# Performance work log

Hardware: AMD Instinct MI355X
Metric: run time of the kernel (lower is better)

The kernel has to match this reference:

```python
import jax, jax.numpy as jnp
import numpy as np

N = 100000   # nodes
E = 1600000  # edges (avg degree 16)
D = 64       # input feature dim


def _lin(k, i, o):
    return (jax.random.normal(k, (i, o), jnp.float32) / np.float32(np.sqrt(i)))


def setup_inputs() -> dict:
    key = jax.random.key(0)
    ks = jax.random.split(key, 12)
    return {
        "x": jax.random.normal(ks[0], (N, D), jnp.float32),
        "edge_index": jax.random.randint(ks[1], (2, E), 0, N, dtype=jnp.int64),
        # layer 1: SAGEConv(64, 64, 'pool')
        "W1_pool": _lin(ks[2], 64, 64), "b1_pool": jnp.zeros((64,), jnp.float32),
        "W1_self": _lin(ks[3], 64, 64), "W1_neigh": _lin(ks[4], 64, 64),
        "b1": jnp.zeros((64,), jnp.float32),
        # layer 2: SAGEConv(64, 32, 'pool')
        "W2_pool": _lin(ks[5], 64, 64), "b2_pool": jnp.zeros((64,), jnp.float32),
        "W2_self": _lin(ks[6], 64, 32), "W2_neigh": _lin(ks[7], 64, 32),
        "b2": jnp.zeros((32,), jnp.float32),
        # layer 3: SAGEConv(32, 32, 'mean')
        "W3_self": _lin(ks[8], 32, 32), "W3_neigh": _lin(ks[9], 32, 32),
        "b3": jnp.zeros((32,), jnp.float32),
    }


def _sage_pool(x, src, dst, Wp, bp, Ws, Wn, b):
    # max-pool aggregator: transform all nodes once (cheaper than per-edge),
    # gather per-edge, segment-max into destination nodes.
    m = jax.nn.relu(x @ Wp + bp)[src]                      # [E, in]
    agg = jax.ops.segment_max(m, dst, num_segments=N)     # [N, in]
    agg = jnp.where(jnp.isfinite(agg), agg, jnp.float32(0.0))  # isolated nodes -> 0
    return x @ Ws + agg @ Wn + b


def _sage_mean(x, src, dst, Ws, Wn, b):
    s = jax.ops.segment_sum(x[src], dst, num_segments=N)   # [N, in]
    cnt = jax.ops.segment_sum(jnp.ones((src.shape[0],), jnp.float32), dst,
                              num_segments=N)
    agg = s / jnp.maximum(cnt, jnp.float32(1.0))[:, None]
    return x @ Ws + agg @ Wn + b


def reference(x, edge_index,
              W1_pool, b1_pool, W1_self, W1_neigh, b1,
              W2_pool, b2_pool, W2_self, W2_neigh, b2,
              W3_self, W3_neigh, b3):
    src, dst = edge_index[0], edge_index[1]
    h = jax.nn.relu(_sage_pool(x, src, dst, W1_pool, b1_pool, W1_self, W1_neigh, b1))
    h = _sage_pool(h, src, dst, W2_pool, b2_pool, W2_self, W2_neigh, b2)
    h = _sage_mean(h, src, dst, W3_self, W3_neigh, b3)
    return h
```

## Files before the change

### kernel.cpp

```cpp
#include <hip/hip_runtime.h>
#include <hip/hip_bf16.h>


typedef unsigned int uint;
typedef short short8 __attribute__((ext_vector_type(8)));
typedef float f32x4 __attribute__((ext_vector_type(4)));
typedef float f32x2 __attribute__((ext_vector_type(2)));
typedef unsigned short u16x8 __attribute__((ext_vector_type(8)));

__device__ __forceinline__ float bf2f(unsigned short h){
  return __uint_as_float(((uint)h) << 16);
}
__device__ __forceinline__ unsigned short f2bf(float f){
  uint u = __float_as_uint(f);
  u += 0x7fffu + ((u >> 16) & 1u);
  return (unsigned short)(u >> 16);
}
__device__ __forceinline__ float lo16(uint u){ return __uint_as_float(u << 16); }
__device__ __forceinline__ float hi16(uint u){ return __uint_as_float(u & 0xffff0000u); }

__device__ __forceinline__ uint4 pkmax4(uint4 a, uint4 b){
  u16x8 x = __builtin_bit_cast(u16x8, a);
  u16x8 y = __builtin_bit_cast(u16x8, b);
  return __builtin_bit_cast(uint4, __builtin_elementwise_max(x, y));
}
__device__ __forceinline__ uint4 shflx4(uint4 a, int off){
  uint4 r;
  r.x = (uint)__shfl_xor((int)a.x, off, 64);
  r.y = (uint)__shfl_xor((int)a.y, off, 64);
  r.z = (uint)__shfl_xor((int)a.z, off, 64);
  r.w = (uint)__shfl_xor((int)a.w, off, 64);
  return r;
}
__device__ __forceinline__ f32x2 b2lo(uint u){
  f32x2 r; r.x = lo16(u); r.y = hi16(u); return r;
}

struct WConv {
  const void* src[13];
  int n[13], isbias[13], Cs[13], K[13], off[13];
};

__global__ void conv_w(WConv wc, unsigned short* wtbase, float* bbase,
                       const unsigned short* x, const int* ei,
                       int* flags, int* ccur, int NB){
  __shared__ int sflags[2];
  int t = threadIdx.x;
  if (t < 64){
    int sane = 0;
    #pragma unroll
    for (int k = 0; k < 4; ++k){
      int e = (x[(t * 4 + k) * 2] >> 7) & 0xff;
      sane += (e >= 118 && e <= 134);
    }
    #pragma unroll
    for (int off = 32; off; off >>= 1) sane += __shfl_down(sane, off, 64);
    unsigned long long b = __ballot(ei[1 + 2 * t] != 0);
    if (t == 0){ sflags[0] = (sane >= 128); sflags[1] = (b == 0ull); }
  }
  __syncthreads();
  int isbf = sflags[0];
  if (blockIdx.x == 0){
    if (t == 0){ flags[0] = sflags[0]; flags[1] = sflags[1]; }
    for (int i = t; i < NB; i += 256) ccur[i] = 0;
  }
  int bt = blockIdx.x, n = wc.n[bt];
  if (wc.isbias[bt]){
    float* d = bbase + wc.off[bt];
    for (int i = t; i < n; i += 256)
      d[i] = isbf ? bf2f(((const unsigned short*)wc.src[bt])[i])
                  : ((const float*)wc.src[bt])[i];
  } else {
    unsigned short* d = wtbase + wc.off[bt];
    int Cs = wc.Cs[bt], K = wc.K[bt], Cm = (1 << Cs) - 1;
    for (int i = t; i < n; i += 256){
      int k = i >> Cs, c = i & Cm;
      unsigned short v = isbf ? ((const unsigned short*)wc.src[bt])[i]
                              : f2bf(((const float*)wc.src[bt])[i]);
      d[c * K + k] = v;
    }
  }
}

__device__ __forceinline__ void load_edge(const void* ei, int E, int is64, int e,
                                          int& s, int& d){
  if (is64){
    const long long* p = (const long long*)ei;
    s = (int)p[e]; d = (int)p[E + e];
  } else {
    const int* p = (const int*)ei;
    s = p[e]; d = p[E + e];
  }
}
__device__ __forceinline__ int load_dst(const void* ei, int E, int is64, int e){
  if (is64) return (int)((const long long*)ei)[E + e];
  return ((const int*)ei)[E + e];
}

__device__ __forceinline__ short8 ld_fragA_bf16(const unsigned short* A, int row,
                                                int K, int koff){
  return *(const short8*)(A + (size_t)row * K + koff);
}
__device__ __forceinline__ short8 ld_fragA_f32(const float* A, int row,
                                               int K, int koff){
  const float* q = A + (size_t)row * K + koff;
  float4 f0 = *(const float4*)q;
  float4 f1 = *(const float4*)(q + 4);
  short8 r;
  r[0] = (short)f2bf(f0.x); r[1] = (short)f2bf(f0.y);
  r[2] = (short)f2bf(f0.z); r[3] = (short)f2bf(f0.w);
  r[4] = (short)f2bf(f1.x); r[5] = (short)f2bf(f1.y);
  r[6] = (short)f2bf(f1.z); r[7] = (short)f2bf(f1.w);
  return r;
}
__device__ __forceinline__ unsigned short f2bf_relu(float f){
  return (unsigned short)(f2bf(fmaxf(f, 0.f)) & 0x7fff);
}

#define CSR_CE 8192

__device__ __forceinline__ void phase1_body(
    const void* __restrict__ ei, const int* __restrict__ flags,
    int* __restrict__ ccur, uint* __restrict__ pairs,
    int E, int N, int NB, int S, int CAP, int blk,
    uint* hist, uint* gbase)
{
  int t = threadIdx.x;
  uint dmask = (1u << S) - 1u;
  int is64 = flags[1];
  int e0 = blk * CSR_CE;
  for (int i = t; i < 1024; i += 256) hist[i] = 0;
  __syncthreads();
  #pragma unroll 4
  for (int it = 0; it < CSR_CE / 256; ++it){
    int e = e0 + it * 256 + t;
    if (e >= E) break;
    int d = load_dst(ei, E, is64, e);
    if ((unsigned)d >= (unsigned)N) continue;
    atomicAdd(&hist[d >> S], 1u);
  }
  __syncthreads();
  for (int b = t; b < NB; b += 256){
    uint c = hist[b];
    if (c) gbase[b] = (uint)atomicAdd(&ccur[b], (int)c);
    hist[b] = 0;
  }
  __syncthreads();
  #pragma unroll 4
  for (int it = 0; it < CSR_CE / 256; ++it){
    int e = e0 + it * 256 + t;
    if (e >= E) break;
    int s, d; load_edge(ei, E, is64, e, s, d);
    if ((unsigned)s >= (unsigned)N || (unsigned)d >= (unsigned)N) continue;
    int b = d >> S;
    uint local = atomicAdd(&hist[b], 1u);
    uint pos = gbase[b] + local;
    if (pos >= (uint)CAP) pos = (uint)CAP - 1;
    pairs[(size_t)b * CAP + pos] = ((uint)s << S) | ((uint)d & dmask);
  }
}


template<int AMODE>
__device__ __forceinline__ void mm1_body(
    const void* __restrict__ Av, const unsigned short* __restrict__ WaT,
    const float* __restrict__ bias, const int* __restrict__ flags,
    unsigned short* __restrict__ out, int N, int blk)
{
  int wid = threadIdx.x >> 6, lane = threadIdx.x & 63;
  int n0 = blk * 32;
  int m = lane & 15, quad = lane >> 4, koq = quad * 8;
  int colbase = wid * 16;
  int rowc0 = min(n0 + m, N - 1);
  int rowc1 = min(n0 + 16 + m, N - 1);
  bool af32 = (AMODE == 2) && (flags[0] == 0);
  f32x4 a0 = {0.f,0.f,0.f,0.f}, a1 = {0.f,0.f,0.f,0.f};
  #pragma unroll
  for (int k0 = 0; k0 < 64; k0 += 32){
    short8 af0 = af32 ? ld_fragA_f32((const float*)Av, rowc0, 64, k0 + koq)
                      : ld_fragA_bf16((const unsigned short*)Av, rowc0, 64, k0 + koq);
    short8 af1 = af32 ? ld_fragA_f32((const float*)Av, rowc1, 64, k0 + koq)
                      : ld_fragA_bf16((const unsigned short*)Av, rowc1, 64, k0 + koq);
    short8 wf = *(const short8*)(WaT + (size_t)(colbase + m) * 64 + k0 + koq);
    a0 = __builtin_amdgcn_mfma_f32_16x16x32_bf16(af0, wf, a0, 0, 0, 0);
    a1 = __builtin_amdgcn_mfma_f32_16x16x32_bf16(af1, wf, a1, 0, 0, 0);
  }
  float bv = bias[colbase + m];
  #pragma unroll
  for (int r = 0; r < 4; ++r){
    int rl = quad * 4 + r;
    if (n0 + rl < N)
      out[(size_t)(n0 + rl) * 64 + colbase + m] = f2bf_relu(a0[r] + bv);
    if (n0 + 16 + rl < N)
      out[(size_t)(n0 + 16 + rl) * 64 + colbase + m] = f2bf_relu(a1[r] + bv);
  }
}

template<int AMODE>
__global__ __launch_bounds__(256) void phase1_mm1(
    const void* __restrict__ ei, const int* __restrict__ flags,
    int* __restrict__ ccur, uint* __restrict__ pairs,
    int E, int N, int NB, int S, int CAP, int nP,
    const void* __restrict__ x, const unsigned short* __restrict__ W1pT,
    const float* __restrict__ b1p, unsigned short* __restrict__ mbuf)
{
  __shared__ uint hist[1024];
  __shared__ uint gbase[1024];
  if ((int)blockIdx.x < nP)
    phase1_body(ei, flags, ccur, pairs, E, N, NB, S, CAP, blockIdx.x, hist, gbase);
  else
    mm1_body<AMODE>(x, W1pT, b1p, flags, mbuf, N, blockIdx.x - nP);
}

__global__ void csr_scan0(const int* __restrict__ ccur, int* __restrict__ cbase,
                          int* __restrict__ rowptrN, int NB, int CAP)
{
  __shared__ int sm[256];
  int t = threadIdx.x;
  int g = (NB + 255) / 256;
  int vb = t * g, v[4], s = 0;
  for (int k = 0; k < g; ++k){
    int i = vb + k; int x = (i < NB) ? min(ccur[i], CAP) : 0; v[k] = x; s += x;
  }
  sm[t] = s; __syncthreads();
  for (int off = 1; off < 256; off <<= 1){
    int x = (t >= off) ? sm[t - off] : 0;
    __syncthreads(); sm[t] += x; __syncthreads();
  }
  int run = sm[t] - s;
  for (int k = 0; k < g; ++k){
    int i = vb + k;
    if (i < NB){ cbase[i] = run; run += v[k]; }
  }
  if (t == 255){ cbase[NB] = run; *rowptrN = run; }
}

#define P2_CAP 6144
__global__ __launch_bounds__(256) void csr_phase2(
    const int* __restrict__ cbase, const int* __restrict__ ccur,
    const uint* __restrict__ pairs,
    int* __restrict__ bucket, int* __restrict__ row_ptr, int N, int S, int CAP)
{
  __shared__ int lbuf[P2_CAP];
  __shared__ int cur[1024];
  __shared__ int sm[256];
  int b = blockIdx.x, t = threadIdx.x;
  uint dmask = (1u << S) - 1u;
  int n0 = b << S;
  int n1 = n0 + (1 << S); if (n1 > N) n1 = N;
  int nn = n1 - n0;
  int base = cbase[b];
  int cnt = min(ccur[b], CAP);
  const uint* bp = pairs + (size_t)b * CAP;

  for (int i = t; i < nn; i += 256) cur[i] = 0;
  __syncthreads();
  for (int j = t; j < cnt; j += 256)
    atomicAdd(&cur[(int)(bp[j] & dmask)], 1);
  __syncthreads();
  int g = (nn + 255) / 256, vb = t * g, v[4], s = 0;
  for (int k = 0; k < g; ++k){
    int i = vb + k; int x = (i < nn) ? cur[i] : 0; v[k] = x; s += x;
  }
  sm[t] = s; __syncthreads();
  for (int off = 1; off < 256; off <<= 1){
    int x = (t >= off) ? sm[t - off] : 0;
    __syncthreads(); sm[t] += x; __syncthreads();
  }
  int run = sm[t] - s;
  for (int k = 0; k < g; ++k){
    int i = vb + k;
    if (i < nn){ row_ptr[n0 + i] = base + run; cur[i] = run; run += v[k]; }
  }
  __syncthreads();
  if (cnt <= 0) return;
  if (cnt <= P2_CAP){
    for (int j = t; j < cnt; j += 256){
      uint pr = bp[j];
      int pos = atomicAdd(&cur[(int)(pr & dmask)], 1);
      lbuf[pos] = (int)(pr >> S);
    }
    __syncthreads();
    for (int i = t; i < cnt; i += 256) bucket[base + i] = lbuf[i];
  } else {
    for (int j = t; j < cnt; j += 256){
      uint pr = bp[j];
      int pos = atomicAdd(&cur[(int)(pr & dmask)], 1);
      bucket[base + pos] = (int)(pr >> S);
    }
  }
}

__device__ __forceinline__ void gmax_pair(
    const int* __restrict__ row_ptr, const int* __restrict__ bucket,
    const unsigned short* __restrict__ m,
    unsigned short* la_row, int LDH, int nodeA, int N, int lane)
{
  int nodeB = nodeA + 1;
  int nAc = min(nodeA, N - 1);
  int rsA = row_ptr[nAc], reA = row_ptr[nAc + 1];
  int cntA = (nodeA < N) ? (reA - rsA) : 0;
  int rsB = reA;
  int cntB = (nodeB < N) ? (row_ptr[nodeB + 1] - reA) : 0;
  int fg8 = (lane & 7) * 8, rowsel = lane >> 3;
  uint4 accA = {0u,0u,0u,0u}, accB = {0u,0u,0u,0u};
  int cmax = max(cntA, cntB);
  for (int c0 = 0; c0 < cmax; c0 += 64){
    int chA = min(cntA - c0, 64);
    int chB = min(cntB - c0, 64);
    int bvA = (lane < chA) ? bucket[rsA + c0 + lane] : 0;
    int bvB = (lane < chB) ? bucket[rsB + c0 + lane] : 0;
    int it = (max(chA, chB) + 7) >> 3;
    int sA = __shfl(bvA, rowsel, 64);
    int sB = __shfl(bvB, rowsel, 64);
    uint4 vA = *(const uint4*)(m + (size_t)sA * 64 + fg8);
    uint4 vB = *(const uint4*)(m + (size_t)sB * 64 + fg8);
    for (int k = 0; k + 1 < it; ++k){
      int jn = (k + 1) * 8 + rowsel;
      int sAn = __shfl(bvA, jn, 64);
      int sBn = __shfl(bvB, jn, 64);
      uint4 nA = *(const uint4*)(m + (size_t)sAn * 64 + fg8);
      uint4 nB = *(const uint4*)(m + (size_t)sBn * 64 + fg8);
      int j = k * 8 + rowsel;
      if (j < chA) accA = pkmax4(accA, vA);
      if (j < chB) accB = pkmax4(accB, vB);
      vA = nA; vB = nB;
    }
    int jl = (it - 1) * 8 + rowsel;
    if (jl < chA) accA = pkmax4(accA, vA);
    if (jl < chB) accB = pkmax4(accB, vB);
  }
  #pragma unroll
  for (int off = 8; off <= 32; off <<= 1){
    accA = pkmax4(accA, shflx4(accA, off));
    accB = pkmax4(accB, shflx4(accB, off));
  }
  if (lane < 8){
    *(uint4*)(la_row + fg8) = accA;
  } else if (lane < 16){
    *(uint4*)(la_row + LDH + (lane & 7) * 8) = accB;
  }
}

template<int AMODE>
__global__ __launch_bounds__(256) void gmax_mm_fused(
    const void* __restrict__ Av, const unsigned short* __restrict__ msrc,
    const int* __restrict__ row_ptr, const int* __restrict__ bucket,
    const unsigned short* __restrict__ WaT, const unsigned short* __restrict__ WbT,
    const float* __restrict__ bias1,
    const unsigned short* __restrict__ WcT, const float* __restrict__ bias2,
    const int* __restrict__ flags,
    unsigned short* __restrict__ out1, unsigned short* __restrict__ out2, int N)
{
  constexpr int K = 64, C = 64, LDH = 72;
  __shared__ unsigned short la[32 * LDH];
  __shared__ unsigned short hl[32 * LDH];
  int wid = threadIdx.x >> 6, lane = threadIdx.x & 63;
  int n0 = blockIdx.x * 32;
  #pragma unroll
  for (int p = 0; p < 4; ++p){
    int lr = wid * 8 + p * 2;
    gmax_pair(row_ptr, bucket, msrc, la + (size_t)lr * LDH, LDH, n0 + lr, N, lane);
  }
  __syncthreads();
  int m = lane & 15, quad = lane >> 4, koq = quad * 8;
  int colbase = wid * 16;
  int rowc0 = min(n0 + m, N - 1);
  int rowc1 = min(n0 + 16 + m, N - 1);
  bool af32 = (AMODE == 2) && (flags[0] == 0);

  f32x4 a0 = {0.f,0.f,0.f,0.f}, a1 = {0.f,0.f,0.f,0.f};
  #pragma unroll
  for (int k0 = 0; k0 < K; k0 += 32){
    short8 af0 = af32 ? ld_fragA_f32((const float*)Av, rowc0, K, k0 + koq)
                      : ld_fragA_bf16((const unsigned short*)Av, rowc0, K, k0 + koq);
    short8 af1 = af32 ? ld_fragA_f32((const float*)Av, rowc1, K, k0 + koq)
                      : ld_fragA_bf16((const unsigned short*)Av, rowc1, K, k0 + koq);
    short8 wf = *(const short8*)(WaT + (size_t)(colbase + m) * K + k0 + koq);
    a0 = __builtin_amdgcn_mfma_f32_16x16x32_bf16(af0, wf, a0, 0, 0, 0);
    a1 = __builtin_amdgcn_mfma_f32_16x16x32_bf16(af1, wf, a1, 0, 0, 0);
    short8 bf0 = *(const short8*)(la + m * LDH + k0 + koq);
    short8 bf1 = *(const short8*)(la + (16 + m) * LDH + k0 + koq);
    short8 wg = *(const short8*)(WbT + (size_t)(colbase + m) * K + k0 + koq);
    a0 = __builtin_amdgcn_mfma_f32_16x16x32_bf16(bf0, wg, a0, 0, 0, 0);
    a1 = __builtin_amdgcn_mfma_f32_16x16x32_bf16(bf1, wg, a1, 0, 0, 0);
  }
  float bv = bias1[colbase + m];
  #pragma unroll
  for (int r = 0; r < 4; ++r){
    int rl = quad * 4 + r;
    unsigned short h0 = f2bf_relu(a0[r] + bv);
    unsigned short h1v = f2bf_relu(a1[r] + bv);
    hl[rl * LDH + colbase + m] = h0;
    hl[(16 + rl) * LDH + colbase + m] = h1v;
    if (n0 + rl < N) out1[(size_t)(n0 + rl) * C + colbase + m] = h0;
    if (n0 + 16 + rl < N) out1[(size_t)(n0 + 16 + rl) * C + colbase + m] = h1v;
  }
  __syncthreads();
  f32x4 c0 = {0.f,0.f,0.f,0.f}, c1 = {0.f,0.f,0.f,0.f};
  #pragma unroll
  for (int k0 = 0; k0 < K; k0 += 32){
    short8 q0 = *(const short8*)(hl + m * LDH + k0 + koq);
    short8 q1 = *(const short8*)(hl + (16 + m) * LDH + k0 + koq);
    short8 wf = *(const short8*)(WcT + (size_t)(colbase + m) * K + k0 + koq);
    c0 = __builtin_amdgcn_mfma_f32_16x16x32_bf16(q0, wf, c0, 0, 0, 0);
    c1 = __builtin_amdgcn_mfma_f32_16x16x32_bf16(q1, wf, c1, 0, 0, 0);
  }
  float b2v = bias2[colbase + m];
  #pragma unroll
  for (int r = 0; r < 4; ++r){
    int rl = quad * 4 + r;
    if (n0 + rl < N)
      out2[(size_t)(n0 + rl) * C + colbase + m] = f2bf_relu(c0[r] + b2v);
    if (n0 + 16 + rl < N)
      out2[(size_t)(n0 + 16 + rl) * C + colbase + m] = f2bf_relu(c1[r] + b2v);
  }
}

__global__ __launch_bounds__(256) void gmax_mm2(
    const unsigned short* __restrict__ h1, const unsigned short* __restrict__ msrc,
    const int* __restrict__ row_ptr, const int* __restrict__ bucket,
    const unsigned short* __restrict__ WsT, const unsigned short* __restrict__ WnT,
    const float* __restrict__ bias, unsigned short* __restrict__ h2, int N)
{
  constexpr int LDH = 72;
  __shared__ unsigned short la[64 * LDH];
  int wid = threadIdx.x >> 6, lane = threadIdx.x & 63;
  int n0 = blockIdx.x * 64;
  #pragma unroll
  for (int p = 0; p < 8; ++p){
    int lr = wid * 16 + p * 2;
    gmax_pair(row_ptr, bucket, msrc, la + (size_t)lr * LDH, LDH, n0 + lr, N, lane);
  }
  __syncthreads();
  int m = lane & 15, quad = lane >> 4, koq = quad * 8;
  int colbase = (wid & 1) * 16;
  int rb = (wid >> 1) * 32;
  int rowc0 = min(n0 + rb + m, N - 1), rowc1 = min(n0 + rb + 16 + m, N - 1);
  f32x4 a0 = {0.f,0.f,0.f,0.f}, a1 = {0.f,0.f,0.f,0.f};
  #pragma unroll
  for (int k0 = 0; k0 < 64; k0 += 32){
    short8 af0 = *(const short8*)(h1 + (size_t)rowc0 * 64 + k0 + koq);
    short8 af1 = *(const short8*)(h1 + (size_t)rowc1 * 64 + k0 + koq);
    short8 wf = *(const short8*)(WsT + (size_t)(colbase + m) * 64 + k0 + koq);
    a0 = __builtin_amdgcn_mfma_f32_16x16x32_bf16(af0, wf, a0, 0, 0, 0);
    a1 = __builtin_amdgcn_mfma_f32_16x16x32_bf16(af1, wf, a1, 0, 0, 0);
    short8 bf0 = *(const short8*)(la + (rb + m) * LDH + k0 + koq);
    short8 bf1 = *(const short8*)(la + (rb + 16 + m) * LDH + k0 + koq);
    short8 wg = *(const short8*)(WnT + (size_t)(colbase + m) * 64 + k0 + koq);
    a0 = __builtin_amdgcn_mfma_f32_16x16x32_bf16(bf0, wg, a0, 0, 0, 0);
    a1 = __builtin_amdgcn_mfma_f32_16x16x32_bf16(bf1, wg, a1, 0, 0, 0);
  }
  float bv = bias[colbase + m];
  #pragma unroll
  for (int r = 0; r < 4; ++r){
    int rl = quad * 4 + r;
    if (n0 + rb + rl < N)
      h2[(size_t)(n0 + rb + rl) * 32 + colbase + m] = f2bf(a0[r] + bv);
    if (n0 + rb + 16 + rl < N)
      h2[(size_t)(n0 + rb + 16 + rl) * 32 + colbase + m] = f2bf(a1[r] + bv);
  }
}

__global__ __launch_bounds__(256) void gsum3(
    const int* __restrict__ row_ptr, const int* __restrict__ bucket,
    const unsigned short* __restrict__ h2,
    const unsigned short* __restrict__ W3sT, const unsigned short* __restrict__ W3nT,
    const float* __restrict__ b3, float* __restrict__ out, int N)
{
  constexpr int LDA = 40;
  __shared__ unsigned short la[16 * LDA];
  int t = threadIdx.x;
  int w = t >> 6, lane = t & 63;
  int n0 = blockIdx.x * 16;
  int g = lane >> 4, q = lane & 15;
  int nd = n0 + w * 4 + g;
  int ndc = nd < N ? nd : N - 1;
  int rs = row_ptr[ndc];
  int cnt = (nd < N) ? (row_ptr[ndc + 1] - rs) : 0;
  int fg8 = (q & 3) * 8, rowsel = q >> 2;
  f32x2 a0 = {0.f,0.f}, a1 = {0.f,0.f}, a2 = {0.f,0.f}, a3 = {0.f,0.f};
  for (int c0 = 0; c0 < cnt; c0 += 16){
    int chunk = min(cnt - c0, 16);
    int bval = (q < chunk) ? bucket[rs + c0 + q] : 0;
    int it = (chunk + 3) >> 2;
    for (int k = 0; k < it; ++k){
      int j = k * 4 + rowsel;
      int s = __shfl(bval, (g << 4) + j, 64);
      uint4 v = *(const uint4*)(h2 + (size_t)s * 32 + fg8);
      if (j < chunk){
        a0 += b2lo(v.x); a1 += b2lo(v.y); a2 += b2lo(v.z); a3 += b2lo(v.w);
      }
    }
  }
  #pragma unroll
  for (int off = 4; off <= 8; off <<= 1){
    a0.x += __shfl_xor(a0.x, off, 64); a0.y += __shfl_xor(a0.y, off, 64);
    a1.x += __shfl_xor(a1.x, off, 64); a1.y += __shfl_xor(a1.y, off, 64);
    a2.x += __shfl_xor(a2.x, off, 64); a2.y += __shfl_xor(a2.y, off, 64);
    a3.x += __shfl_xor(a3.x, off, 64); a3.y += __shfl_xor(a3.y, off, 64);
  }
  if (rowsel == 0){
    float sc = 1.f / fmaxf((float)cnt, 1.f);
    int r = w * 4 + g;
    uint4 pk;
    pk.x = (uint)f2bf(a0.x * sc) | ((uint)f2bf(a0.y * sc) << 16);
    pk.y = (uint)f2bf(a1.x * sc) | ((uint)f2bf(a1.y * sc) << 16);
    pk.z = (uint)f2bf(a2.x * sc) | ((uint)f2bf(a2.y * sc) << 16);
    pk.w = (uint)f2bf(a3.x * sc) | ((uint)f2bf(a3.y * sc) << 16);
    *(uint4*)(la + r * LDA + q * 8) = pk;
  }
  __syncthreads();
  if (w < 2){
    int m = lane & 15, quad = lane >> 4, koq = quad * 8;
    int colbase = w * 16;
    int row = n0 + m;
    int rowc = row < N ? row : N - 1;
    f32x4 acc = {0.f, 0.f, 0.f, 0.f};
    short8 aself = *(const short8*)(h2 + (size_t)rowc * 32 + koq);
    short8 wfs = *(const short8*)(W3sT + (size_t)(colbase + m) * 32 + koq);
    acc = __builtin_amdgcn_mfma_f32_16x16x32_bf16(aself, wfs, acc, 0, 0, 0);
    short8 aagg = *(const short8*)(la + m * LDA + koq);
    short8 wfn = *(const short8*)(W3nT + (size_t)(colbase + m) * 32 + koq);
    acc = __builtin_amdgcn_mfma_f32_16x16x32_bf16(aagg, wfn, acc, 0, 0, 0);
    float bv = b3[colbase + m];
    #pragma unroll
    for (int r = 0; r < 4; ++r){
      int orow = n0 + quad * 4 + r;
      if (orow < N) out[(size_t)orow * 32 + colbase + m] = acc[r] + bv;
    }
  }
}

static inline char* align256(char* p){
  return (char*)(((uintptr_t)p + 255) & ~(uintptr_t)255);
}

extern "C" void kernel_launch(void* const* d_in, const int* in_sizes, int n_in,
                              void* d_out, int out_size, void* d_ws, size_t ws_size,
                              hipStream_t stream)
{
  const void* x = d_in[0];
  const void* ei = d_in[1];
  int N = in_sizes[0] / 64;
  int E = in_sizes[1] / 2;

  char* ws = (char*)d_ws;
  unsigned short* wtbase = (unsigned short*)ws;
  float* bbase = (float*)(ws + 65536);
  int* flags = (int*)(ws + 131072 - 256);

  int S = 7, NB = (N + 127) >> 7;
  while (NB > 1024){ S++; NB = (N + (1 << S) - 1) >> S; }
  int CAP = ((2 * E / NB) + 255) & ~255;
  if (CAP < 1024) CAP = 1024;

  char* p = ws + 131072;
  int* row_ptr = (int*)p; p = align256(p + (size_t)(N + 1) * 4);
  int* cbase   = (int*)p; p = align256(p + 4352);
  int* ccur    = (int*)p; p = align256(p + 4352);
  int* bucket  = (int*)p; p = align256(p + (size_t)E * 4);
  uint* pairs  = (uint*)p; p = align256(p + (size_t)NB * CAP * 4);
  char* P = p;  p = align256(p + (size_t)N * 64 * 2);
  char* Q = p;  p = align256(p + (size_t)N * 64 * 2);
  char* R = p;  p = align256(p + (size_t)N * 64 * 2);
  unsigned short* m1 = (unsigned short*)P;
  unsigned short* h2 = (unsigned short*)P;
  unsigned short* m2 = (unsigned short*)Q;
  unsigned short* h1 = (unsigned short*)R;

  WConv wc;
  {
    const int widx[13] = {2, 3, 4, 5, 6, 7, 8, 9, 10, 11, 12, 13, 14};
    const int isb[13]  = {0, 1, 0, 0, 1, 0, 1, 0, 0, 1, 0, 0, 1};
    const int Cs[13]   = {6, 0, 6, 6, 0, 6, 0, 5, 5, 0, 5, 5, 0};
    const int Kk[13]   = {64, 0, 64, 64, 0, 64, 0, 64, 64, 0, 32, 32, 0};
    const int off[13]  = {0, 0, 4096, 8192, 64, 12288, 128, 16384, 18432, 192,
                          20480, 21504, 224};
    for (int i = 0; i < 13; ++i){
      wc.src[i] = d_in[widx[i]]; wc.n[i] = in_sizes[widx[i]];
      wc.isbias[i] = isb[i]; wc.Cs[i] = Cs[i]; wc.K[i] = Kk[i]; wc.off[i] = off[i];
    }
  }
  hipLaunchKernelGGL(conv_w, dim3(13), dim3(256), 0, stream, wc, wtbase, bbase,
                     (const unsigned short*)x, (const int*)ei, flags, ccur, NB);
  unsigned short* W1pT = wtbase + 0;     unsigned short* W1sT = wtbase + 4096;
  unsigned short* W1nT = wtbase + 8192;  unsigned short* W2pT = wtbase + 12288;
  unsigned short* W2sT = wtbase + 16384; unsigned short* W2nT = wtbase + 18432;
  unsigned short* W3sT = wtbase + 20480; unsigned short* W3nT = wtbase + 21504;
  float* b1p = bbase + 0;  float* b1 = bbase + 64; float* b2p = bbase + 128;
  float* b2 = bbase + 192; float* b3 = bbase + 224;

  int nP = (E + CSR_CE - 1) / CSR_CE;
  int RT32 = (N + 31) / 32;
  int RT16 = (N + 15) / 16;

  phase1_mm1<2><<<nP + RT32, 256, 0, stream>>>(
      ei, flags, ccur, pairs, E, N, NB, S, CAP, nP, x, W1pT, b1p, m1);
  csr_scan0<<<1, 256, 0, stream>>>(ccur, cbase, row_ptr + N, NB, CAP);
  csr_phase2<<<NB, 256, 0, stream>>>(cbase, ccur, pairs, bucket, row_ptr, N, S, CAP);

  gmax_mm_fused<2><<<RT32,256,0,stream>>>(
      x, m1, row_ptr, bucket, W1sT, W1nT, b1, W2pT, b2p, flags, h1, m2, N);

  gmax_mm2<<<(N + 63) / 64,256,0,stream>>>(
      h1, m2, row_ptr, bucket, W2sT, W2nT, b2, h2, N);

  gsum3<<<RT16,256,0,stream>>>(row_ptr, bucket, h2, W3sT, W3nT, b3,
                               (float*)d_out, N);
}
```

Before: 271.9 us.

## Replace atomic bucket reservation with per-block histogram scan and separate placement pass

Edge bucketing no longer reserves space per block with global atomics into fixed-capacity bucket slots. It now writes per-block bucket histograms, does a 2D prefix scan across blocks, and runs a separate placement kernel that writes pairs into a compact, exactly sized array. This removes global atomics and the capacity-clamping risk, and makes placement deterministic. In exchange it adds two kernel launches and reads the edge list a second time in a separate kernel.

Result: slower. 287.7 us (+5.8%).

```diff
diff --git a/kernel.cpp b/kernel.cpp
--- a/kernel.cpp
+++ b/kernel.cpp
@@ -119,14 +119,11 @@
 
 #define CSR_CE 8192
 
-__device__ __forceinline__ void phase1_body(
+__device__ __forceinline__ void count_body(
     const void* __restrict__ ei, const int* __restrict__ flags,
-    int* __restrict__ ccur, uint* __restrict__ pairs,
-    int E, int N, int NB, int S, int CAP, int blk,
-    uint* hist, uint* gbase)
+    int* __restrict__ hcnt, int E, int N, int NB, int S, int blk, uint* hist)
 {
   int t = threadIdx.x;
-  uint dmask = (1u << S) - 1u;
   int is64 = flags[1];
   int e0 = blk * CSR_CE;
   for (int i = t; i < 1024; i += 256) hist[i] = 0;
@@ -140,26 +137,9 @@
     atomicAdd(&hist[d >> S], 1u);
   }
   __syncthreads();
-  for (int b = t; b < NB; b += 256){
-    uint c = hist[b];
-    if (c) gbase[b] = (uint)atomicAdd(&ccur[b], (int)c);
-    hist[b] = 0;
-  }
-  __syncthreads();
-  #pragma unroll 4
-  for (int it = 0; it < CSR_CE / 256; ++it){
-    int e = e0 + it * 256 + t;
-    if (e >= E) break;
-    int s, d; load_edge(ei, E, is64, e, s, d);
-    if ((unsigned)s >= (unsigned)N || (unsigned)d >= (unsigned)N) continue;
-    int b = d >> S;
-    uint local = atomicAdd(&hist[b], 1u);
-    uint pos = gbase[b] + local;
-    if (pos >= (uint)CAP) pos = (uint)CAP - 1;
-    pairs[(size_t)b * CAP + pos] = ((uint)s << S) | ((uint)d & dmask);
-  }
-}
-
+  for (int b = t; b < NB; b += 256)
+    hcnt[blk * 1024 + b] = (int)hist[b];
+}
 
 template<int AMODE>
 __device__ __forceinline__ void mm1_body(
@@ -197,19 +177,32 @@
 }
 
 template<int AMODE>
-__global__ __launch_bounds__(256) void phase1_mm1(
+__global__ __launch_bounds__(256) void count_mm1(
     const void* __restrict__ ei, const int* __restrict__ flags,
-    int* __restrict__ ccur, uint* __restrict__ pairs,
-    int E, int N, int NB, int S, int CAP, int nP,
+    int* __restrict__ hcnt, int E, int N, int NB, int S, int nP,
     const void* __restrict__ x, const unsigned short* __restrict__ W1pT,
     const float* __restrict__ b1p, unsigned short* __restrict__ mbuf)
 {
   __shared__ uint hist[1024];
-  __shared__ uint gbase[1024];
   if ((int)blockIdx.x < nP)
-    phase1_body(ei, flags, ccur, pairs, E, N, NB, S, CAP, blockIdx.x, hist, gbase);
+    count_body(ei, flags, hcnt, E, N, NB, S, blockIdx.x, hist);
   else
     mm1_body<AMODE>(x, W1pT, b1p, flags, mbuf, N, blockIdx.x - nP);
+}
+
+__global__ __launch_bounds__(512) void scan2d(
+    int* __restrict__ hcnt, int* __restrict__ ccur, int nP, int NB)
+{
+  __shared__ int sm[512];
+  int b = blockIdx.x, t = threadIdx.x;
+  int v = (t < nP) ? hcnt[(size_t)t * 1024 + b] : 0;
+  sm[t] = v; __syncthreads();
+  for (int off = 1; off < 512; off <<= 1){
+    int x = (t >= off) ? sm[t - off] : 0;
+    __syncthreads(); sm[t] += x; __syncthreads();
+  }
+  if (t < nP) hcnt[(size_t)t * 1024 + b] = sm[t] - v;
+  if (t == 511) ccur[b] = sm[511];
 }
 
 __global__ void csr_scan0(const int* __restrict__ ccur, int* __restrict__ cbase,
@@ -235,11 +228,39 @@
   if (t == 255){ cbase[NB] = run; *rowptrN = run; }
 }
 
+__global__ __launch_bounds__(256) void place(
+    const void* __restrict__ ei, const int* __restrict__ flags,
+    const int* __restrict__ cbase, const int* __restrict__ hcnt,
+    uint* __restrict__ pairs, int E, int N, int NB, int S)
+{
+  __shared__ int lbase[1024];
+  __shared__ int cur[1024];
+  int blk = blockIdx.x, t = threadIdx.x;
+  uint dmask = (1u << S) - 1u;
+  int is64 = flags[1];
+  for (int b = t; b < NB; b += 256){
+    lbase[b] = cbase[b] + hcnt[(size_t)blk * 1024 + b];
+    cur[b] = 0;
+  }
+  __syncthreads();
+  int e0 = blk * CSR_CE;
+  #pragma unroll 4
+  for (int it = 0; it < CSR_CE / 256; ++it){
+    int e = e0 + it * 256 + t;
+    if (e >= E) break;
+    int s, d; load_edge(ei, E, is64, e, s, d);
+    if ((unsigned)s >= (unsigned)N || (unsigned)d >= (unsigned)N) continue;
+    int b = d >> S;
+    int local = atomicAdd(&cur[b], 1);
+    pairs[lbase[b] + local] = ((uint)s << S) | ((uint)d & dmask);
+  }
+}
+
 #define P2_CAP 6144
 __global__ __launch_bounds__(256) void csr_phase2(
     const int* __restrict__ cbase, const int* __restrict__ ccur,
     const uint* __restrict__ pairs,
-    int* __restrict__ bucket, int* __restrict__ row_ptr, int N, int S, int CAP)
+    int* __restrict__ bucket, int* __restrict__ row_ptr, int N, int S)
 {
   __shared__ int lbuf[P2_CAP];
   __shared__ int cur[1024];
@@ -250,8 +271,8 @@
   int n1 = n0 + (1 << S); if (n1 > N) n1 = N;
   int nn = n1 - n0;
   int base = cbase[b];
-  int cnt = min(ccur[b], CAP);
-  const uint* bp = pairs + (size_t)b * CAP;
+  int cnt = ccur[b];
+  const uint* bp = pairs + base;
 
   for (int i = t; i < nn; i += 256) cur[i] = 0;
   __syncthreads();
@@ -552,15 +573,14 @@
 
   int S = 7, NB = (N + 127) >> 7;
   while (NB > 1024){ S++; NB = (N + (1 << S) - 1) >> S; }
-  int CAP = ((2 * E / NB) + 255) & ~255;
-  if (CAP < 1024) CAP = 1024;
 
   char* p = ws + 131072;
   int* row_ptr = (int*)p; p = align256(p + (size_t)(N + 1) * 4);
   int* cbase   = (int*)p; p = align256(p + 4352);
   int* ccur    = (int*)p; p = align256(p + 4352);
+  int* hcnt    = (int*)p; p = align256(p + (size_t)512 * 1024 * 4);
   int* bucket  = (int*)p; p = align256(p + (size_t)E * 4);
-  uint* pairs  = (uint*)p; p = align256(p + (size_t)NB * CAP * 4);
+  uint* pairs  = (uint*)p; p = align256(p + (size_t)E * 4);
   char* P = p;  p = align256(p + (size_t)N * 64 * 2);
   char* Q = p;  p = align256(p + (size_t)N * 64 * 2);
   char* R = p;  p = align256(p + (size_t)N * 64 * 2);
@@ -595,10 +615,12 @@
   int RT32 = (N + 31) / 32;
   int RT16 = (N + 15) / 16;
 
-  phase1_mm1<2><<<nP + RT32, 256, 0, stream>>>(
-      ei, flags, ccur, pairs, E, N, NB, S, CAP, nP, x, W1pT, b1p, m1);
-  csr_scan0<<<1, 256, 0, stream>>>(ccur, cbase, row_ptr + N, NB, CAP);
-  csr_phase2<<<NB, 256, 0, stream>>>(cbase, ccur, pairs, bucket, row_ptr, N, S, CAP);
+  count_mm1<2><<<nP + RT32, 256, 0, stream>>>(
+      ei, flags, hcnt, E, N, NB, S, nP, x, W1pT, b1p, m1);
+  scan2d<<<NB, 512, 0, stream>>>(hcnt, ccur, nP, NB);
+  csr_scan0<<<1, 256, 0, stream>>>(ccur, cbase, row_ptr + N, NB, E);
+  place<<<nP, 256, 0, stream>>>(ei, flags, cbase, hcnt, pairs, E, N, NB, S);
+  csr_phase2<<<NB, 256, 0, stream>>>(cbase, ccur, pairs, bucket, row_ptr, N, S);
 
   gmax_mm_fused<2><<<RT32,256,0,stream>>>(
       x, m1, row_ptr, bucket, W1sT, W1nT, b1, W2pT, b2p, flags, h1, m2, N);
```
